# Performance work log

Measured on AMD Instinct MI355X. Metric: run time of the kernel, lower is better.

Reference implementation:

```python
import jax, jax.numpy as jnp
import numpy as np

NUM_HEADS = 16

def setup_inputs() -> dict:
    key = jax.random.key(0)
    ks = jax.random.split(key, 5)
    b, s, d = 4, 1024, 1024
    scale = 0.02
    return {
        "x": jax.random.normal(ks[0], (b, s, d), dtype=jnp.float32),
        "Wq": jax.random.normal(ks[1], (d, d), dtype=jnp.float32) * scale,
        "Wk": jax.random.normal(ks[2], (d, d), dtype=jnp.float32) * scale,
        "Wv": jax.random.normal(ks[3], (d, d), dtype=jnp.float32) * scale,
        "Wo": jax.random.normal(ks[4], (d, d), dtype=jnp.float32) * scale,
        "bo": jnp.zeros((d,), dtype=jnp.float32),
    }

def reference(x, Wq, Wk, Wv, Wo, bo):
    b, s, d_in = x.shape
    h = NUM_HEADS
    hd = Wq.shape[0] // h  # head_dim
    # torch Linear: y = x @ W.T ; reshape to [b, s, h, hd] then transpose to [b, h, s, hd]
    q = (x @ Wq.T).reshape(b, s, h, hd).transpose(0, 2, 1, 3)
    k = (x @ Wk.T).reshape(b, s, h, hd).transpose(0, 2, 1, 3)
    v = (x @ Wv.T).reshape(b, s, h, hd).transpose(0, 2, 1, 3)
    # attention scores [b, h, s, s]
    scores = jnp.einsum('bhqd,bhkd->bhqk', q, k)
    # NOTE: the original calls masked_fill (NOT masked_fill_), which returns a
    # new tensor that is discarded -> the causal mask is never actually applied.
    # We faithfully reproduce that: no mask.
    attn = jax.nn.softmax(scores / jnp.sqrt(jnp.float32(hd)), axis=-1)
    # dropout p=0.0 -> identity
    ctx = jnp.einsum('bhqk,bhkd->bhqd', attn, v)  # [b, h, s, hd]
    ctx = ctx.transpose(0, 2, 1, 3).reshape(b, s, h * hd)
    return ctx @ Wo.T + bo
```

## Files before the change

kernel.cpp:

```cpp
#include <hip/hip_runtime.h>
#include <hip/hip_bf16.h>

#define BB 4
#define SS 1024
#define DD 1024
#define HH 16
#define HDIM 64
#define MM (BB*SS)

typedef __attribute__((ext_vector_type(8))) short  bf16x8;
typedef __attribute__((ext_vector_type(4))) float  f32x4v;

static __device__ __forceinline__ unsigned short f2bf(float f) {
    union { float f; unsigned u; } v; v.f = f;
    unsigned r = v.u + 0x7fff + ((v.u >> 16) & 1);
    return (unsigned short)(r >> 16);
}

__global__ __launch_bounds__(256) void qkv_gemm(
    const float* __restrict__ x,
    const float* __restrict__ Wq, const float* __restrict__ Wk, const float* __restrict__ Wv,
    unsigned short* __restrict__ q_ws, unsigned short* __restrict__ k_ws,
    unsigned short* __restrict__ v_ws)
{
    const int bn = blockIdx.x;
    const int bm = blockIdx.y;
    const int bz = blockIdx.z;
    const float* W;
    unsigned short* outp;
    if (bz == 0)      { W = Wq; outp = q_ws; }
    else if (bz == 1) { W = Wk; outp = k_ws; }
    else              { W = Wv; outp = v_ws; }

    const int tid = threadIdx.x;
    const int wid = tid >> 6, lane = tid & 63;
    const int wr = wid >> 1, wc = wid & 1;
    const int lhi = lane >> 4, llo = lane & 15;

    __shared__ unsigned short As[128 * 40];
    __shared__ unsigned short Bs[128 * 40];

    f32x4v acc[4][4] = {};
    const int m0 = bm * 128, n0 = bn * 128;

    for (int kt = 0; kt < DD / 32; ++kt) {
        __syncthreads();
        #pragma unroll
        for (int i = 0; i < 4; ++i) {
            int idx = tid + i * 256;
            int row = idx >> 3, c4 = (idx & 7) * 4;
            f32x4v xv = *(const f32x4v*)(x + (size_t)(m0 + row) * DD + kt * 32 + c4);
            unsigned p0 = (unsigned)f2bf(xv[0]) | ((unsigned)f2bf(xv[1]) << 16);
            unsigned p1 = (unsigned)f2bf(xv[2]) | ((unsigned)f2bf(xv[3]) << 16);
            uint2 pk; pk.x = p0; pk.y = p1;
            *(uint2*)(As + row * 40 + c4) = pk;

            f32x4v wv = *(const f32x4v*)(W + (size_t)(n0 + row) * DD + kt * 32 + c4);
            unsigned q0 = (unsigned)f2bf(wv[0]) | ((unsigned)f2bf(wv[1]) << 16);
            unsigned q1 = (unsigned)f2bf(wv[2]) | ((unsigned)f2bf(wv[3]) << 16);
            uint2 qk; qk.x = q0; qk.y = q1;
            *(uint2*)(Bs + row * 40 + c4) = qk;
        }
        __syncthreads();

        bf16x8 af[4], bfr[4];
        #pragma unroll
        for (int i = 0; i < 4; ++i)
            af[i] = *(const bf16x8*)(As + (wr * 64 + i * 16 + llo) * 40 + lhi * 8);
        #pragma unroll
        for (int i = 0; i < 4; ++i)
            bfr[i] = *(const bf16x8*)(Bs + (wc * 64 + i * 16 + llo) * 40 + lhi * 8);

        #pragma unroll
        for (int i = 0; i < 4; ++i)
            #pragma unroll
            for (int j = 0; j < 4; ++j)
                acc[i][j] = __builtin_amdgcn_mfma_f32_16x16x32_bf16(af[i], bfr[j], acc[i][j], 0, 0, 0);
    }

    #pragma unroll
    for (int i = 0; i < 4; ++i) {
        #pragma unroll
        for (int j = 0; j < 4; ++j) {
            #pragma unroll
            for (int r = 0; r < 4; ++r) {
                int mrow = m0 + wr * 64 + i * 16 + lhi * 4 + r;
                int ncol = n0 + wc * 64 + j * 16 + llo;
                float val = acc[i][j][r];
                size_t idx = ((size_t)((mrow >> 10) * HH + (ncol >> 6)) * SS + (mrow & 1023)) * HDIM + (ncol & 63);
                outp[idx] = f2bf(val);
            }
        }
    }
}

__global__ __launch_bounds__(256) void attn_kernel(
    const unsigned short* __restrict__ q_ws,
    const unsigned short* __restrict__ k_ws,
    const unsigned short* __restrict__ v_ws,
    unsigned short* __restrict__ ctx)
{
    const int qt = blockIdx.x;
    const int bh = blockIdx.y;
    const int tid = threadIdx.x, wid = tid >> 6, lane = tid & 63;
    const int lhi = lane >> 4, llo = lane & 15;

    __shared__ unsigned short Ks[64 * 72];
    __shared__ unsigned short VT[64 * 72];
    __shared__ unsigned short Ps[4][16 * 72];

    const size_t basekv = (size_t)bh * SS * HDIM;
    const int qrow0 = qt * 64 + wid * 16;

    bf16x8 aq[2];
    #pragma unroll
    for (int ks = 0; ks < 2; ++ks)
        aq[ks] = *(const bf16x8*)(q_ws + basekv + (size_t)(qrow0 + llo) * HDIM + ks * 32 + lhi * 8);

    f32x4v o[4] = {};
    float m_run[4], l_run[4];
    #pragma unroll
    for (int j = 0; j < 4; ++j) { m_run[j] = -1e30f; l_run[j] = 0.f; }

    for (int kvt = 0; kvt < 16; ++kvt) {
        __syncthreads();
        #pragma unroll
        for (int i = 0; i < 2; ++i) {
            int idx = tid + i * 256;
            int row = idx >> 3, c8 = (idx & 7) * 8;
            *(bf16x8*)(Ks + row * 72 + c8) =
                *(const bf16x8*)(k_ws + basekv + (size_t)(kvt * 64 + row) * HDIM + c8);
        }
        #pragma unroll
        for (int i = 0; i < 16; ++i) {
            int idx = tid + i * 256;
            int kv = idx >> 6, hd = idx & 63;
            VT[hd * 72 + kv] = v_ws[basekv + (size_t)(kvt * 64 + kv) * HDIM + hd];
        }
        __syncthreads();

        f32x4v s[4] = {};
        #pragma unroll
        for (int ni = 0; ni < 4; ++ni) {
            #pragma unroll
            for (int ks = 0; ks < 2; ++ks) {
                bf16x8 bk = *(const bf16x8*)(Ks + (ni * 16 + llo) * 72 + ks * 32 + lhi * 8);
                s[ni] = __builtin_amdgcn_mfma_f32_16x16x32_bf16(aq[ks], bk, s[ni], 0, 0, 0);
            }
        }
        #pragma unroll
        for (int ni = 0; ni < 4; ++ni) s[ni] = s[ni] * 0.125f;

        #pragma unroll
        for (int j = 0; j < 4; ++j) {
            float tmax = fmaxf(fmaxf(s[0][j], s[1][j]), fmaxf(s[2][j], s[3][j]));
            #pragma unroll
            for (int off = 1; off < 16; off <<= 1)
                tmax = fmaxf(tmax, __shfl_xor(tmax, off, 64));
            float mn = fmaxf(m_run[j], tmax);
            float alpha = __expf(m_run[j] - mn);
            float rs = 0.f;
            #pragma unroll
            for (int ni = 0; ni < 4; ++ni) {
                float p = __expf(s[ni][j] - mn);
                s[ni][j] = p;
                rs += p;
            }
            #pragma unroll
            for (int off = 1; off < 16; off <<= 1)
                rs += __shfl_xor(rs, off, 64);
            l_run[j] = l_run[j] * alpha + rs;
            m_run[j] = mn;
            #pragma unroll
            for (int ni = 0; ni < 4; ++ni) o[ni][j] *= alpha;
        }

        unsigned short* pw = Ps[wid];
        #pragma unroll
        for (int ni = 0; ni < 4; ++ni)
            #pragma unroll
            for (int j = 0; j < 4; ++j)
                pw[(lhi * 4 + j) * 72 + ni * 16 + llo] = f2bf(s[ni][j]);
        asm volatile("s_waitcnt lgkmcnt(0)" ::: "memory");

        #pragma unroll
        for (int ks = 0; ks < 2; ++ks) {
            bf16x8 pa = *(const bf16x8*)(pw + llo * 72 + ks * 32 + lhi * 8);
            #pragma unroll
            for (int ni = 0; ni < 4; ++ni) {
                bf16x8 bv = *(const bf16x8*)(VT + (ni * 16 + llo) * 72 + ks * 32 + lhi * 8);
                o[ni] = __builtin_amdgcn_mfma_f32_16x16x32_bf16(pa, bv, o[ni], 0, 0, 0);
            }
        }
    }

    const int b = bh >> 4, h = bh & 15;
    #pragma unroll
    for (int ni = 0; ni < 4; ++ni) {
        #pragma unroll
        for (int j = 0; j < 4; ++j) {
            int srow = qrow0 + lhi * 4 + j;
            int hd = ni * 16 + llo;
            float val = o[ni][j] / l_run[j];
            ctx[(size_t)(b * SS + srow) * DD + h * HDIM + hd] = f2bf(val);
        }
    }
}

__global__ __launch_bounds__(256) void out_gemm(
    const unsigned short* __restrict__ ctx,
    const float* __restrict__ Wo,
    const float* __restrict__ bo,
    float* __restrict__ out)
{
    const int bn = blockIdx.x;
    const int bm = blockIdx.y;
    const int tid = threadIdx.x;
    const int wid = tid >> 6, lane = tid & 63;
    const int wr = wid >> 1, wc = wid & 1;
    const int lhi = lane >> 4, llo = lane & 15;

    __shared__ unsigned short As[128 * 40];
    __shared__ unsigned short Bs[128 * 40];

    f32x4v acc[4][4] = {};
    const int m0 = bm * 128, n0 = bn * 128;

    for (int kt = 0; kt < DD / 32; ++kt) {
        __syncthreads();
        #pragma unroll
        for (int i = 0; i < 2; ++i) {
            int idx = tid + i * 256;
            int row = idx >> 2, c8 = (idx & 3) * 8;
            *(bf16x8*)(As + row * 40 + c8) =
                *(const bf16x8*)(ctx + (size_t)(m0 + row) * DD + kt * 32 + c8);
        }
        #pragma unroll
        for (int i = 0; i < 4; ++i) {
            int idx = tid + i * 256;
            int row = idx >> 3, c4 = (idx & 7) * 4;
            f32x4v wv = *(const f32x4v*)(Wo + (size_t)(n0 + row) * DD + kt * 32 + c4);
            unsigned q0 = (unsigned)f2bf(wv[0]) | ((unsigned)f2bf(wv[1]) << 16);
            unsigned q1 = (unsigned)f2bf(wv[2]) | ((unsigned)f2bf(wv[3]) << 16);
            uint2 qk; qk.x = q0; qk.y = q1;
            *(uint2*)(Bs + row * 40 + c4) = qk;
        }
        __syncthreads();

        bf16x8 af[4], bfr[4];
        #pragma unroll
        for (int i = 0; i < 4; ++i)
            af[i] = *(const bf16x8*)(As + (wr * 64 + i * 16 + llo) * 40 + lhi * 8);
        #pragma unroll
        for (int i = 0; i < 4; ++i)
            bfr[i] = *(const bf16x8*)(Bs + (wc * 64 + i * 16 + llo) * 40 + lhi * 8);

        #pragma unroll
        for (int i = 0; i < 4; ++i)
            #pragma unroll
            for (int j = 0; j < 4; ++j)
                acc[i][j] = __builtin_amdgcn_mfma_f32_16x16x32_bf16(af[i], bfr[j], acc[i][j], 0, 0, 0);
    }

    #pragma unroll
    for (int j = 0; j < 4; ++j) {
        int ncol = n0 + wc * 64 + j * 16 + llo;
        float bias = bo[ncol];
        #pragma unroll
        for (int i = 0; i < 4; ++i) {
            #pragma unroll
            for (int r = 0; r < 4; ++r) {
                int mrow = m0 + wr * 64 + i * 16 + lhi * 4 + r;
                out[(size_t)mrow * DD + ncol] = acc[i][j][r] + bias;
            }
        }
    }
}

extern "C" void kernel_launch(void* const* d_in, const int* in_sizes, int n_in,
                              void* d_out, int out_size, void* d_ws, size_t ws_size,
                              hipStream_t stream) {
    const float* x  = (const float*)d_in[0];
    const float* Wq = (const float*)d_in[1];
    const float* Wk = (const float*)d_in[2];
    const float* Wv = (const float*)d_in[3];
    const float* Wo = (const float*)d_in[4];
    const float* bo = (const float*)d_in[5];
    float* out = (float*)d_out;

    unsigned short* q_ws = (unsigned short*)d_ws;
    unsigned short* k_ws = q_ws + (size_t)MM * DD;
    unsigned short* v_ws = k_ws + (size_t)MM * DD;
    unsigned short* ctx  = v_ws + (size_t)MM * DD;

    qkv_gemm<<<dim3(8, 32, 3), 256, 0, stream>>>(x, Wq, Wk, Wv, q_ws, k_ws, v_ws);
    attn_kernel<<<dim3(16, 64), 256, 0, stream>>>(q_ws, k_ws, v_ws, ctx);
    out_gemm<<<dim3(8, 32), 256, 0, stream>>>(ctx, Wo, bo, out);
}
```

Before: 251.7 us.

## Pre-convert x to bf16, double-buffer GEMMs and attention with direct LDS loads

```diff
diff --git a/kernel.cpp b/kernel.cpp
--- a/kernel.cpp
+++ b/kernel.cpp
@@ -10,6 +10,7 @@
 
 typedef __attribute__((ext_vector_type(8))) short  bf16x8;
 typedef __attribute__((ext_vector_type(4))) float  f32x4v;
+typedef __attribute__((ext_vector_type(4))) unsigned short u16x4;
 
 static __device__ __forceinline__ unsigned short f2bf(float f) {
     union { float f; unsigned u; } v; v.f = f;
@@ -17,67 +18,105 @@
     return (unsigned short)(r >> 16);
 }
 
+static __device__ __forceinline__ void gload16(const void* g, const void* lds_uniform_base) {
+    __builtin_amdgcn_global_load_lds(
+        (const __attribute__((address_space(1))) unsigned int*)(uintptr_t)g,
+        (__attribute__((address_space(3))) unsigned int*)(uintptr_t)lds_uniform_base,
+        16, 0, 0);
+}
+
+__global__ __launch_bounds__(256) void convert_x(
+    const float* __restrict__ x, unsigned short* __restrict__ xb)
+{
+    size_t i = ((size_t)blockIdx.x * 256 + threadIdx.x) * 4;
+    f32x4v v = *(const f32x4v*)(x + i);
+    u16x4 o;
+    o[0] = f2bf(v[0]); o[1] = f2bf(v[1]); o[2] = f2bf(v[2]); o[3] = f2bf(v[3]);
+    *(u16x4*)(xb + i) = o;
+}
+
 __global__ __launch_bounds__(256) void qkv_gemm(
-    const float* __restrict__ x,
-    const float* __restrict__ Wq, const float* __restrict__ Wk, const float* __restrict__ Wv,
+    const unsigned short* __restrict__ xb,
+    const float* __restrict__ Wq, const float* __restrict__ Wk,
+    const float* __restrict__ Wv,
     unsigned short* __restrict__ q_ws, unsigned short* __restrict__ k_ws,
     unsigned short* __restrict__ v_ws)
 {
-    const int bn = blockIdx.x;
-    const int bm = blockIdx.y;
-    const int bz = blockIdx.z;
-    const float* W;
-    unsigned short* outp;
-    if (bz == 0)      { W = Wq; outp = q_ws; }
-    else if (bz == 1) { W = Wk; outp = k_ws; }
-    else              { W = Wv; outp = v_ws; }
+    const int bn = blockIdx.x, bm = blockIdx.y, bz = blockIdx.z;
+    const float* W = (bz == 0) ? Wq : (bz == 1) ? Wk : Wv;
+    unsigned short* outp = (bz == 0) ? q_ws : (bz == 1) ? k_ws : v_ws;
 
     const int tid = threadIdx.x;
     const int wid = tid >> 6, lane = tid & 63;
     const int wr = wid >> 1, wc = wid & 1;
     const int lhi = lane >> 4, llo = lane & 15;
 
-    __shared__ unsigned short As[128 * 40];
-    __shared__ unsigned short Bs[128 * 40];
+    __shared__ unsigned short As[2][128 * 32];
+    __shared__ unsigned short Bs[2][128 * 32];
+
+    const int m0 = bm * 128, n0 = bn * 128;
+    const int brow = tid >> 1, bhalf = tid & 1;
+
+    auto stageA = [&](int buf, int kt) {
+        #pragma unroll
+        for (int j = 0; j < 2; ++j) {
+            int chunk = j * 256 + wid * 64 + lane;
+            int row = chunk >> 2, sub = chunk & 3;
+            gload16(xb + (size_t)(m0 + row) * DD + kt * 32 + sub * 8,
+                    &As[buf][(j * 256 + wid * 64) * 8]);
+        }
+    };
+    auto loadB = [&](int kt, f32x4v* r) {
+        const float* p = W + (size_t)(n0 + brow) * DD + kt * 32 + bhalf * 16;
+        r[0] = *(const f32x4v*)(p);
+        r[1] = *(const f32x4v*)(p + 4);
+        r[2] = *(const f32x4v*)(p + 8);
+        r[3] = *(const f32x4v*)(p + 12);
+    };
+    auto writeB = [&](int buf, const f32x4v* r) {
+        bf16x8 p0, p1;
+        #pragma unroll
+        for (int e = 0; e < 4; ++e) {
+            p0[e]     = (short)f2bf(r[0][e]);
+            p0[e + 4] = (short)f2bf(r[1][e]);
+            p1[e]     = (short)f2bf(r[2][e]);
+            p1[e + 4] = (short)f2bf(r[3][e]);
+        }
+        *(bf16x8*)&Bs[buf][brow * 32 + bhalf * 16]     = p0;
+        *(bf16x8*)&Bs[buf][brow * 32 + bhalf * 16 + 8] = p1;
+    };
 
     f32x4v acc[4][4] = {};
-    const int m0 = bm * 128, n0 = bn * 128;
-
-    for (int kt = 0; kt < DD / 32; ++kt) {
-        __syncthreads();
-        #pragma unroll
-        for (int i = 0; i < 4; ++i) {
-            int idx = tid + i * 256;
-            int row = idx >> 3, c4 = (idx & 7) * 4;
-            f32x4v xv = *(const f32x4v*)(x + (size_t)(m0 + row) * DD + kt * 32 + c4);
-            unsigned p0 = (unsigned)f2bf(xv[0]) | ((unsigned)f2bf(xv[1]) << 16);
-            unsigned p1 = (unsigned)f2bf(xv[2]) | ((unsigned)f2bf(xv[3]) << 16);
-            uint2 pk; pk.x = p0; pk.y = p1;
-            *(uint2*)(As + row * 40 + c4) = pk;
-
-            f32x4v wv = *(const f32x4v*)(W + (size_t)(n0 + row) * DD + kt * 32 + c4);
-            unsigned q0 = (unsigned)f2bf(wv[0]) | ((unsigned)f2bf(wv[1]) << 16);
-            unsigned q1 = (unsigned)f2bf(wv[2]) | ((unsigned)f2bf(wv[3]) << 16);
-            uint2 qk; qk.x = q0; qk.y = q1;
-            *(uint2*)(Bs + row * 40 + c4) = qk;
-        }
-        __syncthreads();
+    f32x4v br[4];
+
+    stageA(0, 0);
+    loadB(0, br);
+    writeB(0, br);
+    __syncthreads();
+
+    for (int kt = 0; kt < 32; ++kt) {
+        int cur = kt & 1;
+        if (kt < 31) { loadB(kt + 1, br); stageA(cur ^ 1, kt + 1); }
 
         bf16x8 af[4], bfr[4];
         #pragma unroll
         for (int i = 0; i < 4; ++i)
-            af[i] = *(const bf16x8*)(As + (wr * 64 + i * 16 + llo) * 40 + lhi * 8);
-        #pragma unroll
-        for (int i = 0; i < 4; ++i)
-            bfr[i] = *(const bf16x8*)(Bs + (wc * 64 + i * 16 + llo) * 40 + lhi * 8);
+            af[i] = *(const bf16x8*)&As[cur][(wr * 64 + i * 16 + llo) * 32 + lhi * 8];
+        #pragma unroll
+        for (int i = 0; i < 4; ++i)
+            bfr[i] = *(const bf16x8*)&Bs[cur][(wc * 64 + i * 16 + llo) * 32 + lhi * 8];
 
         #pragma unroll
         for (int i = 0; i < 4; ++i)
             #pragma unroll
             for (int j = 0; j < 4; ++j)
                 acc[i][j] = __builtin_amdgcn_mfma_f32_16x16x32_bf16(af[i], bfr[j], acc[i][j], 0, 0, 0);
-    }
-
+
+        if (kt < 31) writeB(cur ^ 1, br);
+        __syncthreads();
+    }
+
+    const float sc = (bz == 0) ? 0.125f : 1.0f;
     #pragma unroll
     for (int i = 0; i < 4; ++i) {
         #pragma unroll
@@ -86,7 +125,7 @@
             for (int r = 0; r < 4; ++r) {
                 int mrow = m0 + wr * 64 + i * 16 + lhi * 4 + r;
                 int ncol = n0 + wc * 64 + j * 16 + llo;
-                float val = acc[i][j][r];
+                float val = acc[i][j][r] * sc;
                 size_t idx = ((size_t)((mrow >> 10) * HH + (ncol >> 6)) * SS + (mrow & 1023)) * HDIM + (ncol & 63);
                 outp[idx] = f2bf(val);
             }
@@ -105,8 +144,8 @@
     const int tid = threadIdx.x, wid = tid >> 6, lane = tid & 63;
     const int lhi = lane >> 4, llo = lane & 15;
 
-    __shared__ unsigned short Ks[64 * 72];
-    __shared__ unsigned short VT[64 * 72];
+    __shared__ unsigned short Ks[2][64 * 64];
+    __shared__ unsigned short Vs[2][64 * 64];
     __shared__ unsigned short Ps[4][16 * 72];
 
     const size_t basekv = (size_t)bh * SS * HDIM;
@@ -117,39 +156,42 @@
     for (int ks = 0; ks < 2; ++ks)
         aq[ks] = *(const bf16x8*)(q_ws + basekv + (size_t)(qrow0 + llo) * HDIM + ks * 32 + lhi * 8);
 
+    auto stage = [&](int buf, int kvt) {
+        #pragma unroll
+        for (int j = 0; j < 2; ++j) {
+            int chunk = j * 256 + wid * 64 + lane;
+            int krow = chunk >> 3, ksub = chunk & 7;
+            gload16(k_ws + basekv + (size_t)(kvt * 64 + krow) * HDIM + ((ksub ^ (krow & 7)) * 8),
+                    &Ks[buf][(j * 256 + wid * 64) * 8]);
+            gload16(v_ws + basekv + (size_t)(kvt * 64 + krow) * HDIM + ksub * 8,
+                    &Vs[buf][(j * 256 + wid * 64) * 8]);
+        }
+    };
+
     f32x4v o[4] = {};
     float m_run[4], l_run[4];
     #pragma unroll
     for (int j = 0; j < 4; ++j) { m_run[j] = -1e30f; l_run[j] = 0.f; }
 
+    stage(0, 0);
+    __syncthreads();
+
     for (int kvt = 0; kvt < 16; ++kvt) {
-        __syncthreads();
-        #pragma unroll
-        for (int i = 0; i < 2; ++i) {
-            int idx = tid + i * 256;
-            int row = idx >> 3, c8 = (idx & 7) * 8;
-            *(bf16x8*)(Ks + row * 72 + c8) =
-                *(const bf16x8*)(k_ws + basekv + (size_t)(kvt * 64 + row) * HDIM + c8);
-        }
-        #pragma unroll
-        for (int i = 0; i < 16; ++i) {
-            int idx = tid + i * 256;
-            int kv = idx >> 6, hd = idx & 63;
-            VT[hd * 72 + kv] = v_ws[basekv + (size_t)(kvt * 64 + kv) * HDIM + hd];
-        }
-        __syncthreads();
-
+        const int cur = kvt & 1;
+        if (kvt < 15) stage(cur ^ 1, kvt + 1);
+
+        const char* kbuf = (const char*)&Ks[cur][0];
         f32x4v s[4] = {};
         #pragma unroll
         for (int ni = 0; ni < 4; ++ni) {
+            int row = ni * 16 + llo;
             #pragma unroll
             for (int ks = 0; ks < 2; ++ks) {
-                bf16x8 bk = *(const bf16x8*)(Ks + (ni * 16 + llo) * 72 + ks * 32 + lhi * 8);
+                int colb = (ks * 64 + lhi * 16) ^ ((llo & 7) << 4);
+                bf16x8 bk = *(const bf16x8*)(kbuf + row * 128 + colb);
                 s[ni] = __builtin_amdgcn_mfma_f32_16x16x32_bf16(aq[ks], bk, s[ni], 0, 0, 0);
             }
         }
-        #pragma unroll
-        for (int ni = 0; ni < 4; ++ni) s[ni] = s[ni] * 0.125f;
 
         #pragma unroll
         for (int j = 0; j < 4; ++j) {
@@ -181,28 +223,41 @@
             #pragma unroll
             for (int j = 0; j < 4; ++j)
                 pw[(lhi * 4 + j) * 72 + ni * 16 + llo] = f2bf(s[ni][j]);
+
         asm volatile("s_waitcnt lgkmcnt(0)" ::: "memory");
-
+        __builtin_amdgcn_sched_barrier(0);
+
+        bf16x8 pa[2];
+        #pragma unroll
+        for (int ks = 0; ks < 2; ++ks)
+            pa[ks] = *(const bf16x8*)(pw + llo * 72 + ks * 32 + lhi * 8);
+
+        const unsigned short* vbuf = &Vs[cur][0];
         #pragma unroll
         for (int ks = 0; ks < 2; ++ks) {
-            bf16x8 pa = *(const bf16x8*)(pw + llo * 72 + ks * 32 + lhi * 8);
             #pragma unroll
             for (int ni = 0; ni < 4; ++ni) {
-                bf16x8 bv = *(const bf16x8*)(VT + (ni * 16 + llo) * 72 + ks * 32 + lhi * 8);
-                o[ni] = __builtin_amdgcn_mfma_f32_16x16x32_bf16(pa, bv, o[ni], 0, 0, 0);
-            }
-        }
+                bf16x8 bv;
+                #pragma unroll
+                for (int e = 0; e < 8; ++e)
+                    bv[e] = (short)vbuf[(ks * 32 + lhi * 8 + e) * 64 + ni * 16 + llo];
+                o[ni] = __builtin_amdgcn_mfma_f32_16x16x32_bf16(pa[ks], bv, o[ni], 0, 0, 0);
+            }
+        }
+        __syncthreads();
     }
 
     const int b = bh >> 4, h = bh & 15;
+    float rinv[4];
+    #pragma unroll
+    for (int j = 0; j < 4; ++j) rinv[j] = 1.0f / l_run[j];
     #pragma unroll
     for (int ni = 0; ni < 4; ++ni) {
         #pragma unroll
         for (int j = 0; j < 4; ++j) {
             int srow = qrow0 + lhi * 4 + j;
             int hd = ni * 16 + llo;
-            float val = o[ni][j] / l_run[j];
-            ctx[(size_t)(b * SS + srow) * DD + h * HDIM + hd] = f2bf(val);
+            ctx[(size_t)(b * SS + srow) * DD + h * HDIM + hd] = f2bf(o[ni][j] * rinv[j]);
         }
     }
 }
@@ -213,53 +268,75 @@
     const float* __restrict__ bo,
     float* __restrict__ out)
 {
-    const int bn = blockIdx.x;
-    const int bm = blockIdx.y;
+    const int bn = blockIdx.x, bm = blockIdx.y;
     const int tid = threadIdx.x;
     const int wid = tid >> 6, lane = tid & 63;
     const int wr = wid >> 1, wc = wid & 1;
     const int lhi = lane >> 4, llo = lane & 15;
 
-    __shared__ unsigned short As[128 * 40];
-    __shared__ unsigned short Bs[128 * 40];
+    __shared__ unsigned short As[2][128 * 32];
+    __shared__ unsigned short Bs[2][128 * 32];
+
+    const int m0 = bm * 128, n0 = bn * 128;
+    const int brow = tid >> 1, bhalf = tid & 1;
+
+    auto stageA = [&](int buf, int kt) {
+        #pragma unroll
+        for (int j = 0; j < 2; ++j) {
+            int chunk = j * 256 + wid * 64 + lane;
+            int row = chunk >> 2, sub = chunk & 3;
+            gload16(ctx + (size_t)(m0 + row) * DD + kt * 32 + sub * 8,
+                    &As[buf][(j * 256 + wid * 64) * 8]);
+        }
+    };
+    auto loadB = [&](int kt, f32x4v* r) {
+        const float* p = Wo + (size_t)(n0 + brow) * DD + kt * 32 + bhalf * 16;
+        r[0] = *(const f32x4v*)(p);
+        r[1] = *(const f32x4v*)(p + 4);
+        r[2] = *(const f32x4v*)(p + 8);
+        r[3] = *(const f32x4v*)(p + 12);
+    };
+    auto writeB = [&](int buf, const f32x4v* r) {
+        bf16x8 p0, p1;
+        #pragma unroll
+        for (int e = 0; e < 4; ++e) {
+            p0[e]     = (short)f2bf(r[0][e]);
+            p0[e + 4] = (short)f2bf(r[1][e]);
+            p1[e]     = (short)f2bf(r[2][e]);
+            p1[e + 4] = (short)f2bf(r[3][e]);
+        }
+        *(bf16x8*)&Bs[buf][brow * 32 + bhalf * 16]     = p0;
+        *(bf16x8*)&Bs[buf][brow * 32 + bhalf * 16 + 8] = p1;
+    };
 
     f32x4v acc[4][4] = {};
-    const int m0 = bm * 128, n0 = bn * 128;
-
-    for (int kt = 0; kt < DD / 32; ++kt) {
-        __syncthreads();
-        #pragma unroll
-        for (int i = 0; i < 2; ++i) {
-            int idx = tid + i * 256;
-            int row = idx >> 2, c8 = (idx & 3) * 8;
-            *(bf16x8*)(As + row * 40 + c8) =
-                *(const bf16x8*)(ctx + (size_t)(m0 + row) * DD + kt * 32 + c8);
-        }
-        #pragma unroll
-        for (int i = 0; i < 4; ++i) {
-            int idx = tid + i * 256;
-            int row = idx >> 3, c4 = (idx & 7) * 4;
-            f32x4v wv = *(const f32x4v*)(Wo + (size_t)(n0 + row) * DD + kt * 32 + c4);
-            unsigned q0 = (unsigned)f2bf(wv[0]) | ((unsigned)f2bf(wv[1]) << 16);
-            unsigned q1 = (unsigned)f2bf(wv[2]) | ((unsigned)f2bf(wv[3]) << 16);
-            uint2 qk; qk.x = q0; qk.y = q1;
-            *(uint2*)(Bs + row * 40 + c4) = qk;
-        }
-        __syncthreads();
+    f32x4v br[4];
+
+    stageA(0, 0);
+    loadB(0, br);
+    writeB(0, br);
+    __syncthreads();
+
+    for (int kt = 0; kt < 32; ++kt) {
+        int cur = kt & 1;
+        if (kt < 31) { loadB(kt + 1, br); stageA(cur ^ 1, kt + 1); }
 
         bf16x8 af[4], bfr[4];
         #pragma unroll
         for (int i = 0; i < 4; ++i)
-            af[i] = *(const bf16x8*)(As + (wr * 64 + i * 16 + llo) * 40 + lhi * 8);
-        #pragma unroll
-        for (int i = 0; i < 4; ++i)
-            bfr[i] = *(const bf16x8*)(Bs + (wc * 64 + i * 16 + llo) * 40 + lhi * 8);
+            af[i] = *(const bf16x8*)&As[cur][(wr * 64 + i * 16 + llo) * 32 + lhi * 8];
+        #pragma unroll
+        for (int i = 0; i < 4; ++i)
+            bfr[i] = *(const bf16x8*)&Bs[cur][(wc * 64 + i * 16 + llo) * 32 + lhi * 8];
 
         #pragma unroll
         for (int i = 0; i < 4; ++i)
             #pragma unroll
             for (int j = 0; j < 4; ++j)
                 acc[i][j] = __builtin_amdgcn_mfma_f32_16x16x32_bf16(af[i], bfr[j], acc[i][j], 0, 0, 0);
+
+        if (kt < 31) writeB(cur ^ 1, br);
+        __syncthreads();
     }
 
     #pragma unroll
@@ -288,12 +365,14 @@
     const float* bo = (const float*)d_in[5];
     float* out = (float*)d_out;
 
-    unsigned short* q_ws = (unsigned short*)d_ws;
+    unsigned short* xb   = (unsigned short*)d_ws;
+    unsigned short* q_ws = xb   + (size_t)MM * DD;
     unsigned short* k_ws = q_ws + (size_t)MM * DD;
     unsigned short* v_ws = k_ws + (size_t)MM * DD;
-    unsigned short* ctx  = v_ws + (size_t)MM * DD;
-
-    qkv_gemm<<<dim3(8, 32, 3), 256, 0, stream>>>(x, Wq, Wk, Wv, q_ws, k_ws, v_ws);
+    unsigned short* ctx  = xb;
+
+    convert_x<<<4096, 256, 0, stream>>>(x, xb);
+    qkv_gemm<<<dim3(8, 32, 3), 256, 0, stream>>>(xb, Wq, Wk, Wv, q_ws, k_ws, v_ws);
     attn_kernel<<<dim3(16, 64), 256, 0, stream>>>(q_ws, k_ws, v_ws, ctx);
     out_gemm<<<dim3(8, 32), 256, 0, stream>>>(ctx, Wo, bo, out);
 }
```

Result: faster. 240.7 us (-4.4%).
